# Kernel optimization log

Measured on AMD Instinct MI355X. Metric: run time of the kernel, lower is better.

## Reference

```python
import jax, jax.numpy as jnp
import numpy as np

B, L, E, V, H, M, O = 16, 64, 256, 16000, 8, 4, 2
DH = E // H
START = 0

def _pe():
    pos = np.arange(L, dtype=np.float32)[:, None]
    div = np.exp(np.arange(0, E, 2, dtype=np.float32) * (-np.log(10000.0) / E))
    pe = np.zeros((L, E), dtype=np.float32)
    pe[:, 0::2] = np.sin(pos * div)
    pe[:, 1::2] = np.cos(pos * div)
    return jnp.asarray(pe)

PE = _pe()  # [L, E] sinusoidal positional encoding (dropout p=0.0)


def setup_inputs() -> dict:
    key = jax.random.key(0)
    ks = jax.random.split(key, 16)
    g = lambda k, sh, sc: jax.random.normal(k, sh, jnp.float32) * sc
    return {
        'noise': jax.random.normal(ks[0], (B, L), jnp.float32),
        'inEmb_W': g(ks[1], (M, L, L), 1.0 / np.sqrt(L)),   # M stacked Linear(L, L), [in,out] layout
        'inEmb_b': jnp.zeros((M, L), jnp.float32),
        'Wq': g(ks[2], (O, E, E), 1.0 / np.sqrt(E)),
        'bq': jnp.zeros((O, E), jnp.float32),
        'Wk': g(ks[3], (O, E, E), 1.0 / np.sqrt(E)),
        'bk': jnp.zeros((O, E), jnp.float32),
        'Wv': g(ks[4], (O, E, E), 1.0 / np.sqrt(E)),
        'bv': jnp.zeros((O, E), jnp.float32),
        'Wo': g(ks[5], (O, E, E), 1.0 / np.sqrt(E)),
        'bo': jnp.zeros((O, E), jnp.float32),
        'ln_g': jnp.ones((O, E), jnp.float32),
        'ln_b': jnp.zeros((O, E), jnp.float32),
        'emb': g(ks[6], (V, E), 1.0),                       # Word2Vec embedding table
        'soft_W': g(ks[7], (E, V), 1.0 / np.sqrt(E)),       # soft head Linear(E, V)
        'soft_b': jnp.zeros((V,), jnp.float32),
    }


def _ln(x, g, b):
    mu = x.mean(-1, keepdims=True)
    var = ((x - mu) ** 2).mean(-1, keepdims=True)
    return (x - mu) / jnp.sqrt(var + 1e-5) * g + b


def _mha_norm(kv, q, Wq, bq, Wk, bk, Wv, bv, Wo, bo, g, b, kmask):
    # MHAwithNorm: attn(query=q, key=kv, value=kv) -> out proj -> residual -> LayerNorm
    Q = (q @ Wq + bq).reshape(B, L, H, DH)
    K = (kv @ Wk + bk).reshape(B, L, H, DH)
    Vh = (kv @ Wv + bv).reshape(B, L, H, DH)
    s = jnp.einsum('bqhd,bkhd->bhqk', Q, K) / np.sqrt(DH)
    s = jnp.where(kmask[None, None, None, :], s, -1e9)  # only the tok generated positions are valid keys
    a = jax.nn.softmax(s, axis=-1)
    o = jnp.einsum('bhqk,bkhd->bqhd', a, Vh).reshape(B, L, E)
    return _ln(o @ Wo + bo + q, g, b)


def _decode(noise, inEmb_W, inEmb_b, Wq, bq, Wk, bk, Wv, bv, Wo, bo, ln_g, ln_b, emb, soft_W, soft_b):
    w = noise
    for i in range(M):
        w = w @ inEmb_W[i] + inEmb_b[i]
    w = jnp.broadcast_to(w[:, :, None], (B, L, E))  # unsqueeze(-1).repeat(1,1,E)

    Y0 = jnp.zeros((B, L, E), jnp.float32).at[:, 0].set(emb[START] + PE[0])

    def step(Y, tok):
        kmask = jnp.arange(L) < tok  # current sequence length == tok
        out = Y
        for i in range(O):  # cross-attn blocks against w[:, :tok]
            out = _mha_norm(w, out, Wq[i], bq[i], Wk[i], bk[i], Wv[i], bv[i], Wo[i], bo[i], ln_g[i], ln_b[i], kmask)
        for i in range(O):  # same blocks reused as self-attn (faithful to source)
            out = _mha_norm(out, out, Wq[i], bq[i], Wk[i], bk[i], Wv[i], bv[i], Wo[i], bo[i], ln_g[i], ln_b[i], kmask)
        logits = out[:, tok - 1] @ soft_W + soft_b
        probs = jax.nn.softmax(logits, axis=-1)
        nxt = jnp.argmax(probs, axis=-1)  # [B]
        Y = Y.at[:, tok].set(emb[nxt] + PE[tok])
        return Y, (nxt, probs)

    _, (toks, probs) = jax.lax.scan(step, Y0, jnp.arange(1, L))
    return toks, probs  # toks [L-1, B] int, probs [L-1, B, V]


def reference(noise, inEmb_W, inEmb_b, Wq, bq, Wk, bk, Wv, bv, Wo, bo, ln_g, ln_b, emb, soft_W, soft_b):
    toks, _ = _decode(noise, inEmb_W, inEmb_b, Wq, bq, Wk, bk, Wv, bv, Wo, bo, ln_g, ln_b, emb, soft_W, soft_b)
    # torch.stack(out_sent[0]): generated token ids of batch element 0, incl. <START>
    return jnp.concatenate([jnp.array([START], dtype=toks.dtype), toks[:, 0]])
```

## Files before the change

### kernel.cpp

```cpp
#include <hip/hip_runtime.h>
#include <stdint.h>


#define NWG 129
#define NWRK 128
#define NT 256

typedef unsigned long long ull;

__device__ __forceinline__ float ld_c(const float* p){
  return __hip_atomic_load(p, __ATOMIC_RELAXED, __HIP_MEMORY_SCOPE_AGENT);
}
__device__ __forceinline__ void st_c(float* p, float v){
  __hip_atomic_store(p, v, __ATOMIC_RELAXED, __HIP_MEMORY_SCOPE_AGENT);
}
__device__ __forceinline__ int ld_fi(const int* p){
  return __hip_atomic_load(p, __ATOMIC_RELAXED, __HIP_MEMORY_SCOPE_AGENT);
}
__device__ __forceinline__ void st_fi(int* p, int v){
  __hip_atomic_store(p, v, __ATOMIC_RELAXED, __HIP_MEMORY_SCOPE_AGENT);
}
__device__ __forceinline__ ull ld_u64(const ull* p){
  return __hip_atomic_load(p, __ATOMIC_RELAXED, __HIP_MEMORY_SCOPE_AGENT);
}
__device__ __forceinline__ void st_u64(ull* p, ull v){
  __hip_atomic_store(p, v, __ATOMIC_RELAXED, __HIP_MEMORY_SCOPE_AGENT);
}

__device__ __forceinline__ float wredsum(float v){
#pragma unroll
  for (int m=32;m;m>>=1) v += __shfl_xor(v,m,64);
  return v;
}
__device__ __forceinline__ float wredmax(float v){
#pragma unroll
  for (int m=32;m;m>>=1) v = fmaxf(v,__shfl_xor(v,m,64));
  return v;
}
__device__ __forceinline__ float g32sum(float v){
#pragma unroll
  for (int m=16;m;m>>=1) v += __shfl_xor(v,m,64);
  return v;
}
__device__ __forceinline__ float g32max(float v){
#pragma unroll
  for (int m=16;m;m>>=1) v = fmaxf(v,__shfl_xor(v,m,64));
  return v;
}
__device__ __forceinline__ ull shflx64(ull v,int m){
  unsigned int lo=(unsigned int)(v&0xffffffffull), hi=(unsigned int)(v>>32);
  lo=__shfl_xor(lo,m,64); hi=__shfl_xor(hi,m,64);
  return (((ull)hi)<<32)|(ull)lo;
}

__device__ __forceinline__ float pe_val(int l, int e){
  int j = e >> 1;
  float dv = expf((float)(2*j) * (-0.035977892078031970f));
  float arg = (float)l * dv;
  return (e & 1) ? cosf(arg) : sinf(arg);
}

__device__ __forceinline__ void a_chain(const float* xrow, float* rrow,
    float* m8, float* redv,
    const float* KAP, const float* BETA, const float* WVEC,
    const float* CC, const float* UT,
    const float* lng, const float* lnb, int tokm, int t){
  const float ISQ = 0.17677669529663687f;
  for (int blk=0; blk<2; blk++){
    const float* src = blk ? rrow : xrow;
    int hh=t>>5, j=t&31;
    float part=0.f;
    for (int jj=j; jj<256; jj+=32) part += src[jj]*KAP[(blk*8+hh)*256+jj];
    part = g32sum(part);
    float alpha = (part + BETA[blk*8+hh]) * ISQ;
    float s1 = (j<tokm)     ? alpha*WVEC[j]    : -3.4e38f;
    float s2 = (j+32<tokm)  ? alpha*WVEC[j+32] : -3.4e38f;
    float mx = g32max(fmaxf(s1,s2));
    float e1 = expf(s1-mx), e2 = expf(s2-mx);
    float sn = e1*((j<tokm)?WVEC[j]:0.f) + e2*((j+32<tokm)?WVEC[j+32]:0.f);
    float sd = e1+e2;
    sn=g32sum(sn); sd=g32sum(sd);
    if (j==0) m8[hh]=sn/sd;
    __syncthreads();
    float x_ = blk ? rrow[t] : xrow[t];
    float z = CC[blk*256+t] + x_;
#pragma unroll
    for (int h2=0;h2<8;h2++) z += m8[h2]*UT[(blk*8+h2)*256+t];
    float ssum=wredsum(z), ssq=wredsum(z*z);
    int lane=t&63, wid=t>>6;
    if (lane==0){ redv[wid]=ssum; redv[4+wid]=ssq; }
    __syncthreads();
    float ts=redv[0]+redv[1]+redv[2]+redv[3];
    float tq=redv[4]+redv[5]+redv[6]+redv[7];
    float mu=ts*(1.f/256.f);
    float var=tq*(1.f/256.f)-mu*mu;
    float rstd=1.f/sqrtf(var+1e-5f);
    float rv=(z-mu)*rstd*lng[blk*256+t]+lnb[blk*256+t];
    __syncthreads();
    rrow[t]=rv;
    __syncthreads();
  }
}

__device__ __forceinline__ void gbar_f(int* arr, int* rel, int ep){
  __syncthreads();
  if (threadIdx.x==0){
    __builtin_amdgcn_fence(__ATOMIC_RELEASE, "agent");
    __hip_atomic_store(arr + blockIdx.x*16, ep, __ATOMIC_RELAXED, __HIP_MEMORY_SCOPE_AGENT);
  }
  if (blockIdx.x==0){
    if (threadIdx.x < NWG){
      while (__hip_atomic_load(arr + threadIdx.x*16, __ATOMIC_RELAXED, __HIP_MEMORY_SCOPE_AGENT) != ep)
        __builtin_amdgcn_s_sleep(1);
    }
    __syncthreads();
    if (threadIdx.x==0)
      __hip_atomic_store(rel, ep, __ATOMIC_RELAXED, __HIP_MEMORY_SCOPE_AGENT);
  }
  if (threadIdx.x==0){
    while (__hip_atomic_load(rel, __ATOMIC_RELAXED, __HIP_MEMORY_SCOPE_AGENT) != ep)
      __builtin_amdgcn_s_sleep(1);
    __builtin_amdgcn_fence(__ATOMIC_ACQUIRE, "agent");
  }
  __syncthreads();
}

__device__ __forceinline__ void gbar_w(int* arr, int* relv, int ep){
  __syncthreads();
  if (threadIdx.x==0){
    st_fi(arr + blockIdx.x*16, ep);
    while (ld_fi(relv + blockIdx.x*16) != ep) __builtin_amdgcn_s_sleep(1);
  }
  __syncthreads();
}

extern "C" __global__ __launch_bounds__(256, 2)
void gen18124_kernel(const float* __restrict__ noise,
                     const float* __restrict__ iw, const float* __restrict__ ib,
                     const float* __restrict__ Wq, const float* __restrict__ bq,
                     const float* __restrict__ Wk, const float* __restrict__ bk,
                     const float* __restrict__ Wv, const float* __restrict__ bv,
                     const float* __restrict__ Wo, const float* __restrict__ bo,
                     const float* __restrict__ lng, const float* __restrict__ lnb,
                     const float* __restrict__ emb, const float* __restrict__ sw,
                     const float* __restrict__ sb,
                     int* __restrict__ out, float* __restrict__ ws)
{
  const float ISQ = 0.17677669529663687f;
  __shared__ float sm[5376];
  __shared__ ull redU[4];
  __shared__ int winS;
  __shared__ int wms;
  extern __shared__ float swl[];

  float* WVEC = ws;
  float* SKC  = ws+64;
  float* SVC  = ws+576;
  float* KAP  = ws+1088;
  float* UT   = ws+5184;
  float* CC   = ws+9280;
  float* BETA = ws+9792;
  int* ARR = (int*)(ws+10080);
  int* REL = (int*)(ws+12144);
  ull* KEY = (ull*)(ws+12160);
  float* Yg  = ws+14208;
  float* R1  = ws+30592;
  float* QB  = ws+46976;
  float* KB  = ws+63360;
  float* VB  = ws+79744;
  float* R2  = ws+96128;
  float* Z2P = ws+112512;
  float* Z3P = ws+243584;
  int* RELV  = (int*)(ws+245632);
  int* RELV2 = (int*)(ws+247680);
  int* Z3F2  = (int*)(ws+249728);

  const int g = blockIdx.x, t = threadIdx.x;
  int ep = 0;

  if (g < NWRK){
    const int base = g*125;
#pragma unroll 8
    for (int i=t; i<256*128; i+=NT){
      int e=i>>7, c=i&127;
      float val = 0.f;
      if (c<125) val = sw[e*16000 + base + c];
      swl[i]=val;
    }
  }

  if (g < NWRK){
    int c0 = 2*g;
    float a0=Wk[t*256+c0],       a1=Wk[t*256+c0+1];
    float a2=Wk[65536+t*256+c0], a3=Wk[65536+t*256+c0+1];
    float a4=Wv[t*256+c0],       a5=Wv[t*256+c0+1];
    float a6=Wv[65536+t*256+c0], a7=Wv[65536+t*256+c0+1];
    a0=wredsum(a0); a1=wredsum(a1); a2=wredsum(a2); a3=wredsum(a3);
    a4=wredsum(a4); a5=wredsum(a5); a6=wredsum(a6); a7=wredsum(a7);
    int lane=t&63, wid=t>>6;
    if (lane==0){
      sm[wid*8+0]=a0; sm[wid*8+1]=a1; sm[wid*8+2]=a2; sm[wid*8+3]=a3;
      sm[wid*8+4]=a4; sm[wid*8+5]=a5; sm[wid*8+6]=a6; sm[wid*8+7]=a7;
    }
    __syncthreads();
    if (t<8){
      float s=sm[t]+sm[8+t]+sm[16+t]+sm[24+t];
      if (t<4) SKC[(t>>1)*256 + c0 + (t&1)] = s;
      else     SVC[((t-4)>>1)*256 + c0 + ((t-4)&1)] = s;
    }
    __syncthreads();
    if (g==0){
      for (int i=t;i<16384;i+=NT) Z3F2[i]=0;
      float* wl = sm+64;
      if (t<64) wl[t] = noise[t];
      __syncthreads();
      for (int i=0;i<4;i++){
        float acc=0.f;
        if (t<64){
          for (int in_=0;in_<64;in_++) acc += wl[in_]*iw[(i*64+in_)*64+t];
          acc += ib[i*64+t];
        }
        __syncthreads();
        if (t<64) wl[t]=acc;
        __syncthreads();
      }
      if (t<64) WVEC[t]=wl[t];
    }
    if (g==1){
      Yg[t] = emb[t] + pe_val(0,t);
      if (t==0) out[0]=0;
    }
  }
  gbar_f(ARR,REL,++ep);

  if (g < NWRK){
    int c0 = 2*g;
    float p00 = bv[t]    *Wo[t*256+c0],        p01 = bv[t]    *Wo[t*256+c0+1];
    float p10 = bv[256+t]*Wo[65536+t*256+c0],  p11 = bv[256+t]*Wo[65536+t*256+c0+1];
    p00=wredsum(p00); p01=wredsum(p01); p10=wredsum(p10); p11=wredsum(p11);
    int lane=t&63, wid=t>>6;
    if (lane==0){ sm[wid*4+0]=p00; sm[wid*4+1]=p01; sm[wid*4+2]=p10; sm[wid*4+3]=p11; }
    __syncthreads();
    if (t<4){
      float s=sm[t]+sm[4+t]+sm[8+t]+sm[12+t];
      int i=t>>1, cl=t&1;
      CC[i*256+c0+cl] = s + bo[i*256+c0+cl];
    }
    if (t<32){
      int i=t>>4, h2=(t>>1)&7, c=c0+(t&1);
      float s=0.f;
      for (int e2=0;e2<32;e2++) s += SVC[i*256+h2*32+e2]*Wo[i*65536+(h2*32+e2)*256+c];
      UT[(i*8+h2)*256+c]=s;
    }
    if (t>=32 && t<64){
      int u=t-32, i=u>>4, h2=(u>>1)&7, e=c0+(u&1);
      float s=0.f;
      for (int c2=0;c2<32;c2++) s += Wq[i*65536+e*256+h2*32+c2]*SKC[i*256+h2*32+c2];
      KAP[(i*8+h2)*256+e]=s;
    }
    if (g==0 && t>=64 && t<80){
      int u=t-64, i=u>>3, h2=u&7;
      float s=0.f;
      for (int c2=0;c2<32;c2++) s += bq[i*256+h2*32+c2]*SKC[i*256+h2*32+c2];
      BETA[i*8+h2]=s;
    }
  }
  gbar_f(ARR,REL,++ep);

  if (g==0){
    float* axr=sm; float* arr=sm+256; float* am8=sm+512; float* ard=sm+528;
    axr[t]=ld_c(&Yg[t]);
    __syncthreads();
    a_chain(axr,arr,am8,ard, KAP,BETA,WVEC,CC,UT,lng,lnb, 1, t);
    st_c(&R1[t], arr[t]);
  }
  gbar_f(ARR,REL,++ep);

  if (g == NWRK){
    for (int tok=1; tok<64; tok++){
      for (int b=0;b<3;b++){
        ++ep;
        if (t < NWRK){ while (ld_fi(ARR + t*16) != ep) {} }
        __syncthreads();
        if (t < NWRK) st_fi(RELV + t*16, ep);
        __syncthreads();
      }
      ++ep;
      if (t < NWRK){ while (ld_fi(ARR + t*16) != ep) {} }
      __syncthreads();
      ull k = 0ull;
      if (t < NWRK) k = ld_u64(KEY + t*8);
#pragma unroll
      for (int m=32;m;m>>=1){
        ull o=shflx64(k,m);
        k = (o>k)? o : k;
      }
      if ((t&63)==0 && t<NWRK) redU[t>>6]=k;
      __syncthreads();
      if (t==0){
        ull kk=redU[0];
        if (redU[1]>kk) kk=redU[1];
        wms = (int)(~(unsigned int)(kk & 0xffffffffull));
      }
      __syncthreads();
      if (t < NWRK) st_fi(RELV2 + t*16, (ep<<14) | wms);
      __syncthreads();
    }
    return;
  }

  const int h  = g&7;
  const int rg = g>>3;

  for (int tok=1; tok<64; tok++){
    const int n = tok-1;

    {
      float* rows4 = sm;
#pragma unroll
      for (int jj=0;jj<4;jj++) rows4[jj*256+t] = ld_c(&R1[(rg+16*jj)*256+t]);
      if (tok>1 && rg==(n&15)){
        float* axr=sm+2700; float* arr2=sm+2956; float* am8=sm+3212; float* ard=sm+3224;
        int v = winS;
        if (h==0 && t==0) out[n]=v;
        axr[t] = emb[v*256+t] + pe_val(n,t);
        if (h==0) st_c(&Yg[n*256+t], axr[t]);
        __syncthreads();
        a_chain(axr,arr2,am8,ard, KAP,BETA,WVEC,CC,UT,lng,lnb, tok, t);
        rows4[(n>>4)*256+t] = arr2[t];
        if (h==0) st_c(&R1[n*256+t], arr2[t]);
      }
      __syncthreads();
      int c=t&31, epp=t>>5;
      const int col=h*32+c;
      float aq[4]={0,0,0,0}, ak[4]={0,0,0,0}, av[4]={0,0,0,0};
#pragma unroll 8
      for (int e=epp*32; e<epp*32+32; e++){
        float wq_=Wq[e*256+col], wk_=Wk[e*256+col], wv_=Wv[e*256+col];
#pragma unroll
        for (int jj=0;jj<4;jj++){ float r=rows4[jj*256+e]; aq[jj]+=r*wq_; ak[jj]+=r*wk_; av[jj]+=r*wv_; }
      }
#pragma unroll
      for (int jj=0;jj<4;jj++){
        aq[jj]+=__shfl_xor(aq[jj],32,64);
        ak[jj]+=__shfl_xor(ak[jj],32,64);
        av[jj]+=__shfl_xor(av[jj],32,64);
      }
      float4* redq=(float4*)(sm+1056); float4* redk=(float4*)(sm+1568); float4* redv4=(float4*)(sm+2080);
      int lane=t&63, wid=t>>6;
      if (lane<32){
        redq[wid*32+lane]=make_float4(aq[0],aq[1],aq[2],aq[3]);
        redk[wid*32+lane]=make_float4(ak[0],ak[1],ak[2],ak[3]);
        redv4[wid*32+lane]=make_float4(av[0],av[1],av[2],av[3]);
      }
      __syncthreads();
      if (t<32){
        float4 A=redq[t],B4=redq[32+t],C4=redq[64+t],D4=redq[96+t];
        float sq[4]={A.x+B4.x+C4.x+D4.x, A.y+B4.y+C4.y+D4.y, A.z+B4.z+C4.z+D4.z, A.w+B4.w+C4.w+D4.w};
        A=redk[t];B4=redk[32+t];C4=redk[64+t];D4=redk[96+t];
        float sk[4]={A.x+B4.x+C4.x+D4.x, A.y+B4.y+C4.y+D4.y, A.z+B4.z+C4.z+D4.z, A.w+B4.w+C4.w+D4.w};
        A=redv4[t];B4=redv4[32+t];C4=redv4[64+t];D4=redv4[96+t];
        float sv[4]={A.x+B4.x+C4.x+D4.x, A.y+B4.y+C4.y+D4.y, A.z+B4.z+C4.z+D4.z, A.w+B4.w+C4.w+D4.w};
        int cc=h*32+t;
        float bq_=bq[cc], bk_=bk[cc], bv_=bv[cc];
#pragma unroll
        for (int jj=0;jj<4;jj++){
          int q_=rg+16*jj;
          if (q_<tok){
            st_c(&QB[q_*256+cc], sq[jj]+bq_);
            st_c(&KB[q_*256+cc], sk[jj]+bk_);
            st_c(&VB[q_*256+cc], sv[jj]+bv_);
          }
        }
      }
    }
    gbar_w(ARR,RELV,++ep);

    {
      float* Ks=sm; float* Vs=sm+2112; float* qrow=sm+4224; float* arow=sm+4352; float* o2s=sm+4608;
      int k=t>>2, f0=(t&3)*8;
      if (k<tok){
#pragma unroll
        for (int i2=0;i2<8;i2++){
          Ks[k*33+f0+i2]=ld_c(&KB[k*256+h*32+f0+i2]);
          Vs[k*33+f0+i2]=ld_c(&VB[k*256+h*32+f0+i2]);
        }
      }
      if (t<128){ int jj=t>>5, c=t&31; int q_=rg+16*jj; if (q_<tok) qrow[jj*32+c]=ld_c(&QB[q_*256+h*32+c]); }
      __syncthreads();
      int w=t>>6, lane=t&63; int q_=rg+16*w; bool ok=q_<tok;
      float sc=-3.4e38f;
      if (ok && lane<tok){
        sc=0.f;
#pragma unroll
        for (int c2=0;c2<32;c2++) sc+=qrow[w*32+c2]*Ks[lane*33+c2];
        sc*=ISQ;
      }
      float mx=wredmax(sc);
      float ex=(ok&&lane<tok)? expf(sc-mx):0.f;
      float sd=wredsum(ex);
      arow[w*64+lane]= ok ? ex/sd : 0.f;
      __syncthreads();
      int j=lane&31, half=lane>>5;
      float oa=0.f;
      if (ok){ for (int k2=half;k2<tok;k2+=2) oa+=arow[w*64+k2]*Vs[k2*33+j]; }
      oa += __shfl_xor(oa,32,64);
      if (lane<32) o2s[w*32+j]=oa;
      __syncthreads();
      float acc[4]={0,0,0,0};
#pragma unroll 8
      for (int j2=0;j2<32;j2++){
        float wv_=Wo[(h*32+j2)*256+t];
#pragma unroll
        for (int jj=0;jj<4;jj++) acc[jj]+=o2s[jj*32+j2]*wv_;
      }
#pragma unroll
      for (int jj=0;jj<4;jj++){ int q2=rg+16*jj; if (q2<tok) st_c(&Z2P[(h*64+q2)*256+t], acc[jj]); }
    }
    gbar_w(ARR,RELV,++ep);

    {
      float* rows4=sm; float* mus=sm+1024;
#pragma unroll
      for (int jj=0;jj<4;jj++){
        int q_=rg+16*jj;
        float z = bo[t] + ld_c(&R1[q_*256+t]);
#pragma unroll
        for (int h2=0;h2<8;h2++) z += ld_c(&Z2P[(h2*64+q_)*256+t]);
        rows4[jj*256+t]=z;
      }
      __syncthreads();
      {
        int w=t>>6, lane=t&63;
        float v0=rows4[w*256+lane], v1=rows4[w*256+64+lane], v2=rows4[w*256+128+lane], v3=rows4[w*256+192+lane];
        float s=v0+v1+v2+v3, sq2=v0*v0+v1*v1+v2*v2+v3*v3;
        s=wredsum(s); sq2=wredsum(sq2);
        if (lane==0){
          float mu=s*(1.f/256.f);
          float var=sq2*(1.f/256.f)-mu*mu;
          mus[w*2]=mu; mus[w*2+1]=1.f/sqrtf(var+1e-5f);
        }
      }
      __syncthreads();
#pragma unroll
      for (int jj=0;jj<4;jj++){
        float mu=mus[jj*2], rstd=mus[jj*2+1];
        float val=(rows4[jj*256+t]-mu)*rstd*lng[t]+lnb[t];
        rows4[jj*256+t]=val;
        int q_=rg+16*jj;
        if (h==0 && q_==n) st_c(&R2[q_*256+t], val);
      }
      __syncthreads();
      int c=t&31, epp=t>>5;
      const int col=h*32+c;
      float aq[4]={0,0,0,0}, ak[4]={0,0,0,0}, av[4]={0,0,0,0};
#pragma unroll 8
      for (int e=epp*32; e<epp*32+32; e++){
        float wq_=Wq[65536+e*256+col], wk_=Wk[65536+e*256+col], wv_=Wv[65536+e*256+col];
#pragma unroll
        for (int jj=0;jj<4;jj++){ float r=rows4[jj*256+e]; aq[jj]+=r*wq_; ak[jj]+=r*wk_; av[jj]+=r*wv_; }
      }
#pragma unroll
      for (int jj=0;jj<4;jj++){
        aq[jj]+=__shfl_xor(aq[jj],32,64);
        ak[jj]+=__shfl_xor(ak[jj],32,64);
        av[jj]+=__shfl_xor(av[jj],32,64);
      }
      float4* redq=(float4*)(sm+1056); float4* redk=(float4*)(sm+1568); float4* redv4=(float4*)(sm+2080);
      int lane=t&63, wid=t>>6;
      if (lane<32){
        redq[wid*32+lane]=make_float4(aq[0],aq[1],aq[2],aq[3]);
        redk[wid*32+lane]=make_float4(ak[0],ak[1],ak[2],ak[3]);
        redv4[wid*32+lane]=make_float4(av[0],av[1],av[2],av[3]);
      }
      __syncthreads();
      if (t<32){
        float4 A=redq[t],B4=redq[32+t],C4=redq[64+t],D4=redq[96+t];
        float sq[4]={A.x+B4.x+C4.x+D4.x, A.y+B4.y+C4.y+D4.y, A.z+B4.z+C4.z+D4.z, A.w+B4.w+C4.w+D4.w};
        A=redk[t];B4=redk[32+t];C4=redk[64+t];D4=redk[96+t];
        float sk[4]={A.x+B4.x+C4.x+D4.x, A.y+B4.y+C4.y+D4.y, A.z+B4.z+C4.z+D4.z, A.w+B4.w+C4.w+D4.w};
        A=redv4[t];B4=redv4[32+t];C4=redv4[64+t];D4=redv4[96+t];
        float sv[4]={A.x+B4.x+C4.x+D4.x, A.y+B4.y+C4.y+D4.y, A.z+B4.z+C4.z+D4.z, A.w+B4.w+C4.w+D4.w};
        int cc=h*32+t;
#pragma unroll
        for (int jj=0;jj<4;jj++){
          int q_=rg+16*jj;
          if (q_<tok){
            st_c(&KB[q_*256+cc], sk[jj]+bk[256+cc]);
            st_c(&VB[q_*256+cc], sv[jj]+bv[256+cc]);
            if (q_==n) st_c(&QB[q_*256+cc], sq[jj]+bq[256+cc]);
          }
        }
      }
    }
    gbar_w(ARR,RELV,++ep);

    {
      float resid = ld_c(&R2[n*256+t]);
      if (g < 8){
        const int hh = g;
        float* Ks=sm; float* Vs=sm+2112; float* qn=sm+4224; float* arow=sm+4352; float* o3s=sm+4608;
        int k=t>>2, f0=(t&3)*8;
        if (k<tok){
#pragma unroll
          for (int i2=0;i2<8;i2++){
            Ks[k*33+f0+i2]=ld_c(&KB[k*256+hh*32+f0+i2]);
            Vs[k*33+f0+i2]=ld_c(&VB[k*256+hh*32+f0+i2]);
          }
        }
        if (t<32) qn[t]=ld_c(&QB[n*256+hh*32+t]);
        __syncthreads();
        int lane=t&63, w=t>>6;
        if (w==0){
          float sc=-3.4e38f;
          if (lane<tok){
            sc=0.f;
#pragma unroll
            for (int c2=0;c2<32;c2++) sc+=qn[c2]*Ks[lane*33+c2];
            sc*=ISQ;
          }
          float mx=wredmax(sc);
          float ex=(lane<tok)? expf(sc-mx):0.f;
          float sd=wredsum(ex);
          arow[lane]=ex/sd;
        }
        __syncthreads();
        if (w==0){
          int j=lane&31, half=lane>>5;
          float oa=0.f;
          for (int k2=half;k2<tok;k2+=2) oa+=arow[k2]*Vs[k2*33+j];
          oa+=__shfl_xor(oa,32,64);
          if (lane<32) o3s[j]=oa;
        }
        __syncthreads();
        float acc=0.f;
#pragma unroll 8
        for (int j2=0;j2<32;j2++) acc+=o3s[j2]*Wo[65536+(hh*32+j2)*256+t];
        st_c(&Z3P[hh*256+t], acc);
        __syncthreads();
        if (t < NWRK) st_fi(Z3F2 + (hh*NWRK + t)*16, tok);
      } else if (g>=64 && g<127){
        const int q = g-64;
        if (q < tok && tok < 63){
          float* axr=sm; float* arr2=sm+256; float* am8=sm+512; float* ard=sm+528;
          axr[t]=ld_c(&Yg[q*256+t]);
          __syncthreads();
          a_chain(axr,arr2,am8,ard, KAP,BETA,WVEC,CC,UT,lng,lnb, tok+1, t);
          st_c(&R1[q*256+t], arr2[t]);
        }
      }
      if (t<8){ while (ld_fi(Z3F2 + (t*NWRK + g)*16) < tok) __builtin_amdgcn_s_sleep(1); }
      __syncthreads();
      float* outn=sm; float* redv=sm+256; float* pp=sm+512;
      float z = bo[256+t] + resid;
#pragma unroll
      for (int h2=0;h2<8;h2++) z += ld_c(&Z3P[h2*256+t]);
      float s=wredsum(z), sq2=wredsum(z*z);
      int lane=t&63, wid=t>>6;
      if (lane==0){ redv[wid]=s; redv[4+wid]=sq2; }
      __syncthreads();
      float ts=redv[0]+redv[1]+redv[2]+redv[3];
      float tq=redv[4]+redv[5]+redv[6]+redv[7];
      float mu=ts*(1.f/256.f);
      float var=tq*(1.f/256.f)-mu*mu;
      float rstd=1.f/sqrtf(var+1e-5f);
      outn[t]=(z-mu)*rstd*lng[256+t]+lnb[256+t];
      __syncthreads();
      const int c = t & 127, half = t >> 7;
      float acc = 0.f;
      if (c < 125){
        const int e0 = half*128;
#pragma unroll 8
        for (int e=e0; e<e0+128; e++) acc += outn[e]*swl[e*128+c];
      }
      if (half==1 && c<125) pp[c]=acc;
      __syncthreads();
      ull key=0ull;
      if (half==0 && c<125){
        int v=g*125+c;
        float a2 = acc + pp[c] + sb[v];
        unsigned int fb=__float_as_uint(a2);
        fb = (fb&0x80000000u)? ~fb : (fb|0x80000000u);
        key=(((ull)fb)<<32) | (ull)(~(unsigned int)v);
      }
#pragma unroll
      for (int m=32;m;m>>=1){
        ull o=shflx64(key,m);
        key = (o>key)? o : key;
      }
      if (lane==0) redU[wid]=key;
      __syncthreads();
      if (t==0){
        ull kk=redU[0];
        if (redU[1]>kk) kk=redU[1];
        if (redU[2]>kk) kk=redU[2];
        if (redU[3]>kk) kk=redU[3];
        st_u64(KEY + g*8, kk);
      }
    }
    {
      ++ep;
      __syncthreads();
      if (t==0){
        st_fi(ARR + g*16, ep);
        int r;
        while (((r = ld_fi(RELV2 + g*16)) >> 14) != ep) __builtin_amdgcn_s_sleep(1);
        winS = r & 0x3fff;
      }
      __syncthreads();
    }
  }

  if (g==0 && t==0) out[63] = winS;
}

extern "C" void kernel_launch(void* const* d_in, const int* in_sizes, int n_in,
                              void* d_out, int out_size, void* d_ws, size_t ws_size,
                              hipStream_t stream)
{
  (void)in_sizes; (void)n_in; (void)out_size; (void)ws_size;
  hipLaunchKernelGGL(gen18124_kernel, dim3(NWG), dim3(NT), 131072, stream,
    (const float*)d_in[0],  (const float*)d_in[1],  (const float*)d_in[2],
    (const float*)d_in[3],  (const float*)d_in[4],  (const float*)d_in[5],
    (const float*)d_in[6],  (const float*)d_in[7],  (const float*)d_in[8],
    (const float*)d_in[9],  (const float*)d_in[10], (const float*)d_in[11],
    (const float*)d_in[12], (const float*)d_in[13], (const float*)d_in[14],
    (const float*)d_in[15], (int*)d_out, (float*)d_ws);
}
```

Baseline: 4.050 ms.

## Fold final LayerNorm affine into soft-head weights and vectorize K/V loads

Pre-scales the per-block slice of the soft-head weights by the LayerNorm gain and precomputes per-column sums and a constant term (LN bias projected through the weights plus the output bias). The per-step logit then becomes rstd*(raw dot - mu*S1) + const, so the normalized row no longer has to be written before the matvec and one barrier is removed. K/V tile loads in the attention phases also switch to 64-bit atomic loads. This adds one-time setup work per workgroup and changes floating-point rounding, which could flip argmax ties.

```diff
diff --git a/kernel.cpp b/kernel.cpp
--- a/kernel.cpp
+++ b/kernel.cpp
@@ -148,6 +148,8 @@
 {
   const float ISQ = 0.17677669529663687f;
   __shared__ float sm[5376];
+  __shared__ float S1s[128];
+  __shared__ float CONSTs[128];
   __shared__ ull redU[4];
   __shared__ int winS;
   __shared__ int wms;
@@ -184,12 +186,26 @@
     for (int i=t; i<256*128; i+=NT){
       int e=i>>7, c=i&127;
       float val = 0.f;
-      if (c<125) val = sw[e*16000 + base + c];
+      if (c<125) val = lng[256+e]*sw[e*16000 + base + c];
       swl[i]=val;
     }
+    __syncthreads();
+    if (t < 128){
+      float s1v=0.f, cov=0.f;
+      if (t < 125){
+        const int col = base + t;
+        for (int e=0;e<256;e++){
+          s1v += swl[e*128+t];
+          cov += lnb[256+e]*sw[e*16000+col];
+        }
+        cov += sb[col];
+      }
+      S1s[t]=s1v; CONSTs[t]=cov;
+    }
   }
 
   if (g < NWRK){
+    __syncthreads();
     int c0 = 2*g;
     float a0=Wk[t*256+c0],       a1=Wk[t*256+c0+1];
     float a2=Wk[65536+t*256+c0], a3=Wk[65536+t*256+c0+1];
@@ -380,10 +396,17 @@
       float* Ks=sm; float* Vs=sm+2112; float* qrow=sm+4224; float* arow=sm+4352; float* o2s=sm+4608;
       int k=t>>2, f0=(t&3)*8;
       if (k<tok){
-#pragma unroll
-        for (int i2=0;i2<8;i2++){
-          Ks[k*33+f0+i2]=ld_c(&KB[k*256+h*32+f0+i2]);
-          Vs[k*33+f0+i2]=ld_c(&VB[k*256+h*32+f0+i2]);
+        const ull* KBp = (const ull*)(KB + k*256 + h*32 + f0);
+        const ull* VBp = (const ull*)(VB + k*256 + h*32 + f0);
+        ull kb[4], vb[4];
+#pragma unroll
+        for (int i2=0;i2<4;i2++){ kb[i2]=ld_u64(KBp+i2); vb[i2]=ld_u64(VBp+i2); }
+#pragma unroll
+        for (int i2=0;i2<4;i2++){
+          Ks[k*33+f0+2*i2]   = __uint_as_float((unsigned)kb[i2]);
+          Ks[k*33+f0+2*i2+1] = __uint_as_float((unsigned)(kb[i2]>>32));
+          Vs[k*33+f0+2*i2]   = __uint_as_float((unsigned)vb[i2]);
+          Vs[k*33+f0+2*i2+1] = __uint_as_float((unsigned)(vb[i2]>>32));
         }
       }
       if (t<128){ int jj=t>>5, c=t&31; int q_=rg+16*jj; if (q_<tok) qrow[jj*32+c]=ld_c(&QB[q_*256+h*32+c]); }
@@ -502,10 +525,17 @@
         float* Ks=sm; float* Vs=sm+2112; float* qn=sm+4224; float* arow=sm+4352; float* o3s=sm+4608;
         int k=t>>2, f0=(t&3)*8;
         if (k<tok){
-#pragma unroll
-          for (int i2=0;i2<8;i2++){
-            Ks[k*33+f0+i2]=ld_c(&KB[k*256+hh*32+f0+i2]);
-            Vs[k*33+f0+i2]=ld_c(&VB[k*256+hh*32+f0+i2]);
+          const ull* KBp = (const ull*)(KB + k*256 + hh*32 + f0);
+          const ull* VBp = (const ull*)(VB + k*256 + hh*32 + f0);
+          ull kb[4], vb[4];
+#pragma unroll
+          for (int i2=0;i2<4;i2++){ kb[i2]=ld_u64(KBp+i2); vb[i2]=ld_u64(VBp+i2); }
+#pragma unroll
+          for (int i2=0;i2<4;i2++){
+            Ks[k*33+f0+2*i2]   = __uint_as_float((unsigned)kb[i2]);
+            Ks[k*33+f0+2*i2+1] = __uint_as_float((unsigned)(kb[i2]>>32));
+            Vs[k*33+f0+2*i2]   = __uint_as_float((unsigned)vb[i2]);
+            Vs[k*33+f0+2*i2+1] = __uint_as_float((unsigned)(vb[i2]>>32));
           }
         }
         if (t<32) qn[t]=ld_c(&QB[n*256+hh*32+t]);
@@ -555,6 +585,7 @@
       float z = bo[256+t] + resid;
 #pragma unroll
       for (int h2=0;h2<8;h2++) z += ld_c(&Z3P[h2*256+t]);
+      outn[t]=z;
       float s=wredsum(z), sq2=wredsum(z*z);
       int lane=t&63, wid=t>>6;
       if (lane==0){ redv[wid]=s; redv[4+wid]=sq2; }
@@ -564,8 +595,6 @@
       float mu=ts*(1.f/256.f);
       float var=tq*(1.f/256.f)-mu*mu;
       float rstd=1.f/sqrtf(var+1e-5f);
-      outn[t]=(z-mu)*rstd*lng[256+t]+lnb[256+t];
-      __syncthreads();
       const int c = t & 127, half = t >> 7;
       float acc = 0.f;
       if (c < 125){
@@ -578,7 +607,7 @@
       ull key=0ull;
       if (half==0 && c<125){
         int v=g*125+c;
-        float a2 = acc + pp[c] + sb[v];
+        float a2 = rstd*(acc + pp[c] - mu*S1s[c]) + CONSTs[c];
         unsigned int fb=__float_as_uint(a2);
         fb = (fb&0x80000000u)? ~fb : (fb|0x80000000u);
         key=(((ull)fb)<<32) | (ull)(~(unsigned int)v);
```

New measurement: 3.561 ms. 12.1% less time.
